# Optimization experiments

Hardware: AMD Instinct MI355X
Metric: run time of the kernel (lower is better)

Reference implementation:

```python
import jax, jax.numpy as jnp
import numpy as np

N = 50000  # nodes
E = 1600000  # directed edges
F_IN = 64
H = 64
C = 16
EPS = 1e-12


def setup_inputs() -> dict:
    key = jax.random.key(0)
    ks = jax.random.split(key, 10)
    x = jax.random.normal(ks[0], (N, F_IN), jnp.float32)
    edge_index = jax.random.randint(ks[1], (2, E), 0, N, dtype=jnp.int32)
    def lin(k, fan_in, fan_out):
        return jax.random.normal(k, (fan_in, fan_out), jnp.float32) * (1.0 / np.sqrt(fan_in))
    return {
        "x": x,
        "edge_index": edge_index,
        "W1": lin(ks[2], F_IN, H), "b1": jnp.zeros((H,), jnp.float32),
        "W2": lin(ks[3], H, H),    "b2": jnp.zeros((H,), jnp.float32),
        "W3": lin(ks[4], H, H),    "b3": jnp.zeros((H,), jnp.float32),
        "Wlin": lin(ks[5], 3 * H, C), "blin": jnp.zeros((C,), jnp.float32),
    }


def _gcn_norm(edge_index, n):
    # add self loops, compute symmetric GCN normalization D^-1/2 (A+I) D^-1/2
    loop = jnp.arange(n, dtype=edge_index.dtype)
    row = jnp.concatenate([edge_index[0], loop])  # target nodes
    col = jnp.concatenate([edge_index[1], loop])  # source nodes
    deg = jax.ops.segment_sum(jnp.ones_like(row, dtype=jnp.float32), row, num_segments=n)
    dis = jnp.where(deg > 0, jax.lax.rsqrt(jnp.maximum(deg, 1.0)), 0.0)
    norm = dis[row] * dis[col]  # [E+N]
    return row, col, norm


def _gcn_layer(x, row, col, norm, W, b):
    h = x @ W                              # [N, H]
    msg = h[col] * norm[:, None]           # gather sources, scale
    agg = jax.ops.segment_sum(msg, row, num_segments=x.shape[0])  # scatter-add
    return agg + b


def _l2norm(x):
    # torch F.normalize(p=2, dim=1)
    n = jnp.sqrt(jnp.sum(x * x, axis=1, keepdims=True))
    return x / jnp.maximum(n, EPS)


def reference(x, edge_index, W1, b1, W2, b2, W3, b3, Wlin, blin):
    row, col, norm = _gcn_norm(edge_index, x.shape[0])
    stack = []
    h = x
    for (W, b) in ((W1, b1), (W2, b2), (W3, b3)):
        h = _gcn_layer(h, row, col, norm, W, b)
        h = jax.nn.relu(h)
        h = _l2norm(h)
        stack.append(h)
    emb = jnp.concatenate(stack, axis=1)   # [N, 3H]
    out = emb @ Wlin + blin                # [N, C]
    return jax.nn.log_softmax(out, axis=1)
```

## Files before the change

kernel.cpp:

```cpp
#include <hip/hip_runtime.h>
#include <hip/hip_bf16.h>

#define NN 50000
#define EE 1600000
#define NB 391
#define CAPB 4608
#define CPAD 16
#define EPB 2048
#define BCAP 14

typedef __attribute__((ext_vector_type(8))) short short8;
typedef __attribute__((ext_vector_type(4))) float floatx4;

__device__ __forceinline__ float ldext(const void* p, long i, int f32) {
    return f32 ? ((const float*)p)[i]
               : __bfloat162float(((const __hip_bfloat16*)p)[i]);
}

__device__ __forceinline__ float b2f(unsigned short u) {
    unsigned int x = ((unsigned int)u) << 16;
    float f; __builtin_memcpy(&f, &x, 4); return f;
}
__device__ __forceinline__ unsigned short f2b(float f) {
    __hip_bfloat16 h = __float2bfloat16(f);
    unsigned short u; __builtin_memcpy(&u, &h, 2); return u;
}
__device__ __forceinline__ float asf(unsigned int x) {
    float f; __builtin_memcpy(&f, &x, 4); return f;
}

__global__ void k_detect(const unsigned short* __restrict__ xu, int* __restrict__ flag,
                         int* __restrict__ bcur) {
    __shared__ int cnt;
    if (threadIdx.x == 0) cnt = 0;
    __syncthreads();
    for (int k = threadIdx.x; k < NB * CPAD; k += 256) bcur[k] = 0;
    int local = 0;
    for (int j = 0; j < 16; ++j) {
        unsigned short u = xu[2 * (threadIdx.x + 256 * j)];
        int ex = (u >> 7) & 0xFF;
        if (ex == 0xFF || ex < 0x60) local++;
    }
    atomicAdd(&cnt, local);
    __syncthreads();
    if (threadIdx.x == 0) flag[0] = (cnt > 256) ? 1 : 0;
}

__global__ void k_bucket(const int* __restrict__ row, const int* __restrict__ col,
                         int* __restrict__ bcur, unsigned int* __restrict__ bdata) {
    __shared__ int lcnt[NB];
    __shared__ unsigned binned[NB * BCAP];
    int tid = threadIdx.x;
    long base = (long)blockIdx.x * EPB;
    int nedge = (int)min((long)EPB, (long)EE - base);
    for (int k = tid; k < NB; k += 256) lcnt[k] = 0;
    __syncthreads();
    for (int j = tid; j < nedge; j += 256) {
        int r = row[base + j], c = col[base + j];
        int b = r >> 7;
        unsigned rec = ((unsigned)(r & 127) << 16) | (unsigned)c;
        int p = atomicAdd(&lcnt[b], 1);
        if (p < BCAP) binned[b * BCAP + p] = rec;
        else {
            int gp = atomicAdd(&bcur[b * CPAD], 1);
            if (gp < CAPB) bdata[(long)b * CAPB + gp] = rec;
        }
    }
    __syncthreads();
    for (int b = tid; b < NB; b += 256) {
        int n = min(lcnt[b], BCAP);
        if (!n) continue;
        int gb = atomicAdd(&bcur[b * CPAD], n);
        long dst = (long)b * CAPB;
        for (int j = 0; j < n; ++j)
            if (gb + j < CAPB) bdata[dst + gb + j] = binned[b * BCAP + j];
    }
}

__global__ void k_csr(const int* __restrict__ bcur, const unsigned* __restrict__ bdata,
                      int* __restrict__ row_ptr, float* __restrict__ dis,
                      unsigned short* __restrict__ csr_col) {
    __shared__ int cnt[128];
    __shared__ int incl[128];
    __shared__ int curs[128];
    __shared__ int redu[4];
    int b = blockIdx.x, tid = threadIdx.x;
    int lane = tid & 63, wid = tid >> 6;
    int part = 0;
    for (int j = tid; j < b; j += 256) part += min(bcur[j * CPAD], CAPB);
    #pragma unroll
    for (int off = 32; off; off >>= 1) part += __shfl_xor(part, off);
    if (lane == 0) redu[wid] = part;
    if (tid < 128) cnt[tid] = 0;
    __syncthreads();
    int base = redu[0] + redu[1] + redu[2] + redu[3];
    int n = min(bcur[b * CPAD], CAPB);
    const unsigned* dp = bdata + (long)b * CAPB;
    for (int i = tid; i < n; i += 256)
        atomicAdd(&cnt[(dp[i] >> 16) & 127], 1);
    __syncthreads();
    if (tid < 128) {
        int x = cnt[tid];
        #pragma unroll
        for (int off = 1; off < 64; off <<= 1) {
            int y = __shfl_up(x, off);
            if (lane >= off) x += y;
        }
        incl[tid] = x;
    }
    __syncthreads();
    int r0 = b << 7;
    if (tid < 128) {
        int ic = incl[tid] + (wid == 1 ? incl[63] : 0);
        int excl = base + ic - cnt[tid];
        curs[tid] = excl;
        int r = r0 + tid;
        if (r <= NN) row_ptr[r] = excl;
        if (r < NN) dis[r] = rsqrtf((float)(cnt[tid] + 1));
    }
    __syncthreads();
    for (int i = tid; i < n; i += 256) {
        unsigned rec = dp[i];
        int p = atomicAdd(&curs[(rec >> 16) & 127], 1);
        csr_col[p] = (unsigned short)(rec & 0xFFFF);
    }
}

template <bool EXT>
__global__ void k_gemm(const void* __restrict__ X, const void* __restrict__ W,
                       const int* __restrict__ flag, const float* __restrict__ dis,
                       unsigned short* __restrict__ Hout) {
    __shared__ __align__(16) unsigned short xs[64 * 72];
    int tid = threadIdx.x;
    int n0 = blockIdx.x * 64;
    const int f32 = flag[0];
    for (int idx = tid; idx < 4096; idx += 256) {
        int nn = idx >> 6, k = idx & 63;
        int n = n0 + nn;
        unsigned short v = 0;
        if (n < NN) {
            long ofs = (long)n * 64 + k;
            if (EXT) v = f32 ? f2b(((const float*)X)[ofs]) : ((const unsigned short*)X)[ofs];
            else     v = ((const unsigned short*)X)[ofs];
        }
        xs[nn * 72 + k] = v;
    }
    __syncthreads();
    int lane = tid & 63, wid = tid >> 6;
    int m0 = wid * 16;
    int quad = lane >> 4, nl = lane & 15;
    short8 a0 = *(const short8*)(xs + (m0 + nl) * 72 + quad * 8);
    short8 a1 = *(const short8*)(xs + (m0 + nl) * 72 + quad * 8 + 32);
    floatx4 acc[4];
    const unsigned short* Wb = (const unsigned short*)W;
    const float* Wf = (const float*)W;
    #pragma unroll
    for (int ct = 0; ct < 4; ++ct) {
        short8 b0, b1;
        int n = ct * 16 + nl;
        #pragma unroll
        for (int j = 0; j < 8; ++j) {
            int k0 = quad * 8 + j;
            b0[j] = (short)(f32 ? f2b(Wf[k0 * 64 + n]) : Wb[k0 * 64 + n]);
            b1[j] = (short)(f32 ? f2b(Wf[(k0 + 32) * 64 + n]) : Wb[(k0 + 32) * 64 + n]);
        }
        floatx4 c = {0.f, 0.f, 0.f, 0.f};
        c = __builtin_amdgcn_mfma_f32_16x16x32_bf16(a0, b0, c, 0, 0, 0);
        c = __builtin_amdgcn_mfma_f32_16x16x32_bf16(a1, b1, c, 0, 0, 0);
        acc[ct] = c;
    }
    #pragma unroll
    for (int r = 0; r < 4; ++r) {
        int node = n0 + m0 + quad * 4 + r;
        if (node < NN) {
            float dn = dis[node];
            #pragma unroll
            for (int ct = 0; ct < 4; ++ct)
                Hout[(long)node * 64 + ct * 16 + nl] = f2b(dn * acc[ct][r]);
        }
    }
}

__global__ void k_agg(const uint4* __restrict__ hp128, const int* __restrict__ row_ptr,
                      const unsigned short* __restrict__ csr_col,
                      const float* __restrict__ dis, const void* __restrict__ bias,
                      const int* __restrict__ flag,
                      unsigned short* __restrict__ eo ) {
    int lane = threadIdx.x & 63, wid = threadIdx.x >> 6;
    int half = lane >> 5;
    int i = blockIdx.x * 8 + wid * 2 + half;
    bool valid = (i < NN);
    int iv = valid ? i : 0;
    int q4 = (lane >> 3) & 3;
    int fl = lane & 7;
    float2 A0 = {0,0}, A1 = {0,0}, A2 = {0,0}, A3 = {0,0};
    #define ADDU(u) do { \
        A0.x += asf((u).x << 16); A0.y += asf((u).x & 0xFFFF0000u); \
        A1.x += asf((u).y << 16); A1.y += asf((u).y & 0xFFFF0000u); \
        A2.x += asf((u).z << 16); A2.y += asf((u).z & 0xFFFF0000u); \
        A3.x += asf((u).w << 16); A3.y += asf((u).w & 0xFFFF0000u); } while (0)
    if (valid && q4 == 0) {
        uint4 u = hp128[(long)iv * 8 + fl];
        ADDU(u);
    }
    int e  = valid ? row_ptr[iv] : 0;
    int e1 = valid ? row_ptr[iv + 1] : 0;
    while (e + 15 < e1) {
        int c0 = csr_col[e + q4];
        int c1 = csr_col[e + 4 + q4];
        int c2 = csr_col[e + 8 + q4];
        int c3 = csr_col[e + 12 + q4];
        uint4 u0 = hp128[(long)c0 * 8 + fl];
        uint4 u1 = hp128[(long)c1 * 8 + fl];
        uint4 u2 = hp128[(long)c2 * 8 + fl];
        uint4 u3 = hp128[(long)c3 * 8 + fl];
        ADDU(u0); ADDU(u1); ADDU(u2); ADDU(u3);
        e += 16;
    }
    if (e + 7 < e1) {
        int c0 = csr_col[e + q4];
        int c1 = csr_col[e + 4 + q4];
        uint4 u0 = hp128[(long)c0 * 8 + fl];
        uint4 u1 = hp128[(long)c1 * 8 + fl];
        ADDU(u0); ADDU(u1);
        e += 8;
    }
    if (e + 3 < e1) {
        int c = csr_col[e + q4];
        uint4 u = hp128[(long)c * 8 + fl];
        ADDU(u);
        e += 4;
    }
    int rem = e1 - e;
    if (q4 < rem) {
        int c = csr_col[e + q4];
        uint4 u = hp128[(long)c * 8 + fl];
        ADDU(u);
    }
    #undef ADDU
    #pragma unroll
    for (int off = 8; off < 32; off <<= 1) {
        A0.x += __shfl_xor(A0.x, off); A0.y += __shfl_xor(A0.y, off);
        A1.x += __shfl_xor(A1.x, off); A1.y += __shfl_xor(A1.y, off);
        A2.x += __shfl_xor(A2.x, off); A2.y += __shfl_xor(A2.y, off);
        A3.x += __shfl_xor(A3.x, off); A3.y += __shfl_xor(A3.y, off);
    }
    const int f32 = flag[0];
    float di = dis[iv];
    float v0 = fmaf(di, A0.x, ldext(bias, 8 * fl + 0, f32));
    float v1 = fmaf(di, A0.y, ldext(bias, 8 * fl + 1, f32));
    float v2 = fmaf(di, A1.x, ldext(bias, 8 * fl + 2, f32));
    float v3 = fmaf(di, A1.y, ldext(bias, 8 * fl + 3, f32));
    float v4 = fmaf(di, A2.x, ldext(bias, 8 * fl + 4, f32));
    float v5 = fmaf(di, A2.y, ldext(bias, 8 * fl + 5, f32));
    float v6 = fmaf(di, A3.x, ldext(bias, 8 * fl + 6, f32));
    float v7 = fmaf(di, A3.y, ldext(bias, 8 * fl + 7, f32));
    v0 = fmaxf(v0, 0.f); v1 = fmaxf(v1, 0.f); v2 = fmaxf(v2, 0.f); v3 = fmaxf(v3, 0.f);
    v4 = fmaxf(v4, 0.f); v5 = fmaxf(v5, 0.f); v6 = fmaxf(v6, 0.f); v7 = fmaxf(v7, 0.f);
    float s = fmaf(v0, v0, fmaf(v1, v1, fmaf(v2, v2, v3 * v3)))
            + fmaf(v4, v4, fmaf(v5, v5, fmaf(v6, v6, v7 * v7)));
    #pragma unroll
    for (int off = 4; off; off >>= 1) s += __shfl_xor(s, off);
    float inv = 1.f / fmaxf(sqrtf(s), 1e-12f);
    if (valid && q4 == 0) {
        union { unsigned short us[8]; uint4 v; } pk;
        pk.us[0] = f2b(v0 * inv); pk.us[1] = f2b(v1 * inv);
        pk.us[2] = f2b(v2 * inv); pk.us[3] = f2b(v3 * inv);
        pk.us[4] = f2b(v4 * inv); pk.us[5] = f2b(v5 * inv);
        pk.us[6] = f2b(v6 * inv); pk.us[7] = f2b(v7 * inv);
        *(uint4*)(eo + (long)i * 64 + 8 * fl) = pk.v;
    }
}

__global__ void k_out(const unsigned short* __restrict__ emb, const void* __restrict__ Wlin,
                      const void* __restrict__ blin, const int* __restrict__ flag,
                      void* __restrict__ out) {
    __shared__ __align__(16) float Wl[192 * 16];
    __shared__ __align__(16) float es[16 * 196];
    __shared__ float bl[16];
    int tid = threadIdx.x;
    int n0 = blockIdx.x * 16;
    const int f32 = flag[0];
    for (int idx = tid; idx < 3072; idx += 256)
        Wl[idx] = ldext(Wlin, idx, f32);
    if (tid < 16) bl[tid] = ldext(blin, tid, f32);
    for (int idx = tid; idx < 3072; idx += 256) {
        int nn = idx / 192, t = idx - nn * 192;
        int layer = t >> 6, k = t & 63;
        es[nn * 196 + t] = b2f(emb[(long)layer * NN * 64 + (long)(n0 + nn) * 64 + k]);
    }
    __syncthreads();
    int node = tid >> 4, c = tid & 15;
    float acc = bl[c];
    const float* er = es + node * 196;
    for (int k = 0; k < 192; k += 4) {
        float4 ev = *(const float4*)(er + k);
        acc = fmaf(ev.x, Wl[(k + 0) * 16 + c], acc);
        acc = fmaf(ev.y, Wl[(k + 1) * 16 + c], acc);
        acc = fmaf(ev.z, Wl[(k + 2) * 16 + c], acc);
        acc = fmaf(ev.w, Wl[(k + 3) * 16 + c], acc);
    }
    float m = acc;
    #pragma unroll
    for (int off = 8; off; off >>= 1) m = fmaxf(m, __shfl_xor(m, off, 16));
    float ex = __expf(acc - m);
    float s = ex;
    #pragma unroll
    for (int off = 8; off; off >>= 1) s += __shfl_xor(s, off, 16);
    float o = (acc - m) - __logf(s);
    long oidx = (long)(n0 + node) * 16 + c;
    if (f32) ((float*)out)[oidx] = o;
    else     ((__hip_bfloat16*)out)[oidx] = __float2bfloat16(o);
}

extern "C" void kernel_launch(void* const* d_in, const int* in_sizes, int n_in,
                              void* d_out, int out_size, void* d_ws, size_t ws_size,
                              hipStream_t stream) {
    const void* x    = d_in[0];
    const int*  ei   = (const int*)d_in[1];
    const void* W1   = d_in[2];
    const void* b1   = d_in[3];
    const void* W2   = d_in[4];
    const void* b2   = d_in[5];
    const void* W3   = d_in[6];
    const void* b3   = d_in[7];
    const void* Wlin = d_in[8];
    const void* blin = d_in[9];

    unsigned short* h   = (unsigned short*)d_ws;
    unsigned short* emb = h + (long)NN * 64;
    float* dis     = (float*)(emb + (long)3 * NN * 64);
    int*   row_ptr = (int*)(dis + NN);
    int*   flag    = row_ptr + NN + 64;
    int*   bcur    = flag + 16;
    unsigned* bdata = (unsigned*)(bcur + NB * CPAD);
    unsigned short* csr_col = (unsigned short*)(bdata + (long)NB * CAPB);

    const int* row = ei;
    const int* col = ei + EE;

    k_detect<<<1, 256, 0, stream>>>((const unsigned short*)x, flag, bcur);
    k_bucket<<<(EE + EPB - 1) / EPB, 256, 0, stream>>>(row, col, bcur, bdata);
    k_csr<<<NB, 256, 0, stream>>>(bcur, bdata, row_ptr, dis, csr_col);

    int gb = (NN + 63) / 64;
    int ga = (NN + 7) / 8;
    const uint4* hp128 = (const uint4*)h;
    k_gemm<true><<<gb, 256, 0, stream>>>(x, W1, flag, dis, h);
    k_agg<<<ga, 256, 0, stream>>>(hp128, row_ptr, csr_col, dis, b1, flag, emb);
    k_gemm<false><<<gb, 256, 0, stream>>>(emb, W2, flag, dis, h);
    k_agg<<<ga, 256, 0, stream>>>(hp128, row_ptr, csr_col, dis, b2, flag, emb + (long)NN * 64);
    k_gemm<false><<<gb, 256, 0, stream>>>(emb + (long)NN * 64, W3, flag, dis, h);
    k_agg<<<ga, 256, 0, stream>>>(hp128, row_ptr, csr_col, dis, b3, flag, emb + (long)2 * NN * 64);

    k_out<<<NN / 16, 256, 0, stream>>>(emb, Wlin, blin, flag, d_out);
}
```

Measured before the change: 320.5 us.

## Use MFMA for output head, fold detect into bucket, vectorize edge loads

The output projection and log-softmax kernel now uses bf16 16x16x32 MFMA, with one wave per 16 nodes and no shared-memory staging. The separate detect kernel is merged into block 0 of the bucket kernel, and bucket counter zeroing moves to hipMemsetAsync. Edge indices are read as int4 vectors. These changes aim to cut launch count and time in the output kernel. The trade-off is that Wlin is rounded to bf16 when inputs are fp32, and the flag is now written inside the bucket kernel, which is still safe because only later kernels read it.

```diff
diff --git a/kernel.cpp b/kernel.cpp
--- a/kernel.cpp
+++ b/kernel.cpp
@@ -29,41 +29,45 @@
     float f; __builtin_memcpy(&f, &x, 4); return f;
 }
 
-__global__ void k_detect(const unsigned short* __restrict__ xu, int* __restrict__ flag,
-                         int* __restrict__ bcur) {
-    __shared__ int cnt;
-    if (threadIdx.x == 0) cnt = 0;
-    __syncthreads();
-    for (int k = threadIdx.x; k < NB * CPAD; k += 256) bcur[k] = 0;
-    int local = 0;
-    for (int j = 0; j < 16; ++j) {
-        unsigned short u = xu[2 * (threadIdx.x + 256 * j)];
-        int ex = (u >> 7) & 0xFF;
-        if (ex == 0xFF || ex < 0x60) local++;
-    }
-    atomicAdd(&cnt, local);
-    __syncthreads();
-    if (threadIdx.x == 0) flag[0] = (cnt > 256) ? 1 : 0;
-}
-
 __global__ void k_bucket(const int* __restrict__ row, const int* __restrict__ col,
-                         int* __restrict__ bcur, unsigned int* __restrict__ bdata) {
+                         int* __restrict__ bcur, unsigned int* __restrict__ bdata,
+                         const unsigned short* __restrict__ xu, int* __restrict__ flag) {
     __shared__ int lcnt[NB];
     __shared__ unsigned binned[NB * BCAP];
+    __shared__ int dcnt;
     int tid = threadIdx.x;
+    if (blockIdx.x == 0) {
+        if (tid == 0) dcnt = 0;
+        __syncthreads();
+        int local = 0;
+        for (int j = 0; j < 16; ++j) {
+            unsigned short u = xu[2 * (tid + 256 * j)];
+            int ex = (u >> 7) & 0xFF;
+            if (ex == 0xFF || ex < 0x60) local++;
+        }
+        atomicAdd(&dcnt, local);
+        __syncthreads();
+        if (tid == 0) flag[0] = (dcnt > 256) ? 1 : 0;
+    }
     long base = (long)blockIdx.x * EPB;
     int nedge = (int)min((long)EPB, (long)EE - base);
     for (int k = tid; k < NB; k += 256) lcnt[k] = 0;
     __syncthreads();
-    for (int j = tid; j < nedge; j += 256) {
-        int r = row[base + j], c = col[base + j];
-        int b = r >> 7;
-        unsigned rec = ((unsigned)(r & 127) << 16) | (unsigned)c;
-        int p = atomicAdd(&lcnt[b], 1);
-        if (p < BCAP) binned[b * BCAP + p] = rec;
-        else {
-            int gp = atomicAdd(&bcur[b * CPAD], 1);
-            if (gp < CAPB) bdata[(long)b * CAPB + gp] = rec;
+    const int4* r4 = (const int4*)(row + base);
+    const int4* c4 = (const int4*)(col + base);
+    for (int j = tid; j < (nedge >> 2); j += 256) {
+        int4 rr = r4[j], cc = c4[j];
+        #pragma unroll
+        for (int t = 0; t < 4; ++t) {
+            int r = (&rr.x)[t], c = (&cc.x)[t];
+            int b = r >> 7;
+            unsigned rec = ((unsigned)(r & 127) << 16) | (unsigned)c;
+            int p = atomicAdd(&lcnt[b], 1);
+            if (p < BCAP) binned[b * BCAP + p] = rec;
+            else {
+                int gp = atomicAdd(&bcur[b * CPAD], 1);
+                if (gp < CAPB) bdata[(long)b * CAPB + gp] = rec;
+            }
         }
     }
     __syncthreads();
@@ -275,42 +279,45 @@
 __global__ void k_out(const unsigned short* __restrict__ emb, const void* __restrict__ Wlin,
                       const void* __restrict__ blin, const int* __restrict__ flag,
                       void* __restrict__ out) {
-    __shared__ __align__(16) float Wl[192 * 16];
-    __shared__ __align__(16) float es[16 * 196];
-    __shared__ float bl[16];
-    int tid = threadIdx.x;
-    int n0 = blockIdx.x * 16;
+    int tid = threadIdx.x, lane = tid & 63, wid = tid >> 6;
+    int quad = lane >> 4, nl = lane & 15;
+    int base = blockIdx.x * 64 + wid * 16;
     const int f32 = flag[0];
-    for (int idx = tid; idx < 3072; idx += 256)
-        Wl[idx] = ldext(Wlin, idx, f32);
-    if (tid < 16) bl[tid] = ldext(blin, tid, f32);
-    for (int idx = tid; idx < 3072; idx += 256) {
-        int nn = idx / 192, t = idx - nn * 192;
-        int layer = t >> 6, k = t & 63;
-        es[nn * 196 + t] = b2f(emb[(long)layer * NN * 64 + (long)(n0 + nn) * 64 + k]);
-    }
-    __syncthreads();
-    int node = tid >> 4, c = tid & 15;
-    float acc = bl[c];
-    const float* er = es + node * 196;
-    for (int k = 0; k < 192; k += 4) {
-        float4 ev = *(const float4*)(er + k);
-        acc = fmaf(ev.x, Wl[(k + 0) * 16 + c], acc);
-        acc = fmaf(ev.y, Wl[(k + 1) * 16 + c], acc);
-        acc = fmaf(ev.z, Wl[(k + 2) * 16 + c], acc);
-        acc = fmaf(ev.w, Wl[(k + 3) * 16 + c], acc);
-    }
-    float m = acc;
-    #pragma unroll
-    for (int off = 8; off; off >>= 1) m = fmaxf(m, __shfl_xor(m, off, 16));
-    float ex = __expf(acc - m);
-    float s = ex;
-    #pragma unroll
-    for (int off = 8; off; off >>= 1) s += __shfl_xor(s, off, 16);
-    float o = (acc - m) - __logf(s);
-    long oidx = (long)(n0 + node) * 16 + c;
-    if (f32) ((float*)out)[oidx] = o;
-    else     ((__hip_bfloat16*)out)[oidx] = __float2bfloat16(o);
+    const unsigned short* Wb = (const unsigned short*)Wlin;
+    const float* Wf = (const float*)Wlin;
+    int ia = min(base + nl, NN - 1);
+    floatx4 c = {0.f, 0.f, 0.f, 0.f};
+    #pragma unroll
+    for (int kc = 0; kc < 6; ++kc) {
+        short8 b;
+        #pragma unroll
+        for (int j = 0; j < 8; ++j) {
+            int k = kc * 32 + quad * 8 + j;
+            b[j] = (short)(f32 ? f2b(Wf[k * 16 + nl]) : Wb[k * 16 + nl]);
+        }
+        int L = kc >> 1, ko = (kc & 1) * 32 + quad * 8;
+        short8 a = *(const short8*)(emb + (long)L * NN * 64 + (long)ia * 64 + ko);
+        c = __builtin_amdgcn_mfma_f32_16x16x32_bf16(a, b, c, 0, 0, 0);
+    }
+    float bl = ldext(blin, nl, f32);
+    #pragma unroll
+    for (int r = 0; r < 4; ++r) {
+        float v = c[r] + bl;
+        float m = v;
+        #pragma unroll
+        for (int off = 1; off < 16; off <<= 1) m = fmaxf(m, __shfl_xor(m, off));
+        float ex = __expf(v - m);
+        float s = ex;
+        #pragma unroll
+        for (int off = 1; off < 16; off <<= 1) s += __shfl_xor(s, off);
+        float o = (v - m) - __logf(s);
+        int node = base + quad * 4 + r;
+        if (node < NN) {
+            long oidx = (long)node * 16 + nl;
+            if (f32) ((float*)out)[oidx] = o;
+            else     ((__hip_bfloat16*)out)[oidx] = __float2bfloat16(o);
+        }
+    }
 }
 
 extern "C" void kernel_launch(void* const* d_in, const int* in_sizes, int n_in,
@@ -339,8 +346,9 @@
     const int* row = ei;
     const int* col = ei + EE;
 
-    k_detect<<<1, 256, 0, stream>>>((const unsigned short*)x, flag, bcur);
-    k_bucket<<<(EE + EPB - 1) / EPB, 256, 0, stream>>>(row, col, bcur, bdata);
+    (void)hipMemsetAsync(bcur, 0, NB * CPAD * sizeof(int), stream);
+    k_bucket<<<(EE + EPB - 1) / EPB, 256, 0, stream>>>(row, col, bcur, bdata,
+                                                       (const unsigned short*)x, flag);
     k_csr<<<NB, 256, 0, stream>>>(bcur, bdata, row_ptr, dis, csr_col);
 
     int gb = (NN + 63) / 64;
@@ -353,5 +361,5 @@
     k_gemm<false><<<gb, 256, 0, stream>>>(emb + (long)NN * 64, W3, flag, dis, h);
     k_agg<<<ga, 256, 0, stream>>>(hp128, row_ptr, csr_col, dis, b3, flag, emb + (long)2 * NN * 64);
 
-    k_out<<<NN / 16, 256, 0, stream>>>(emb, Wlin, blin, flag, d_out);
-}
+    k_out<<<gb, 256, 0, stream>>>(emb, Wlin, blin, flag, d_out);
+}
```

After: 299.6 us. -6.5%, faster.
